# Performance work log

Hardware: AMD Instinct MI355X
Metric: run time of the kernel (lower is better)

The kernel has to match this reference:

```python
import jax, jax.numpy as jnp
import numpy as np

HEADS = 16

def setup_inputs() -> dict:
    key = jax.random.key(0)
    k1, k2, k3, k4 = jax.random.split(key, 4)
    B, T, S, W = 2, 2048, 2048, 1024
    x = jax.random.normal(k1, (B, T, W), dtype=jnp.float32)
    cond_k = jax.random.normal(k2, (B, S, W), dtype=jnp.float32)
    cond_v = jax.random.normal(k3, (B, S, W), dtype=jnp.float32)
    w_proj = jax.random.normal(k4, (W, W), dtype=jnp.float32) * 0.02
    b_proj = jnp.zeros((W,), dtype=jnp.float32)
    return {"x": x, "cond_k": cond_k, "cond_v": cond_v, "w_proj": w_proj, "b_proj": b_proj}

def reference(x, cond_k, cond_v, w_proj, b_proj):
    B, T, W = x.shape
    S = cond_k.shape[1]
    H = HEADS
    d = W // H
    scale = 1.0 / jnp.sqrt(jnp.sqrt(jnp.float32(d)))  # applied to both q and k
    q = x.reshape(B, T, H, d) * scale
    k = cond_k.reshape(B, S, H, d) * scale
    v = cond_v.reshape(B, S, H, d)
    # scores: [B, H, T, S]
    scores = jnp.einsum('bthd,bshd->bhts', q, k)
    w = jax.nn.softmax(scores.astype(jnp.float32), axis=-1).astype(scores.dtype)
    out = jnp.einsum('bhts,bshd->bthd', w, v).reshape(B, T, W)
    # c_proj: torch Linear -> x @ W.T + b
    return out @ w_proj.T + b_proj
```

## Files before the change

kernel.cpp:

```cpp
#include <hip/hip_runtime.h>

#define Bn 2
#define Hn 16
#define Tn 2048
#define Sn 2048
#define Wd 1024
#define Dh 64

typedef __attribute__((ext_vector_type(8))) short s16x8;
typedef __attribute__((ext_vector_type(4))) short s16x4;
typedef __attribute__((ext_vector_type(4))) float f32x4;
typedef __attribute__((ext_vector_type(4))) unsigned u32x4;

#define MFMA(a, b, c) __builtin_amdgcn_mfma_f32_16x16x32_bf16((a), (b), (c), 0, 0, 0)

__device__ __forceinline__ s16x8 ld8(const short* p) { return *(const s16x8*)p; }

__device__ __forceinline__ short f2bf(float f) {
    unsigned u = __builtin_bit_cast(unsigned, f);
    u += 0x7FFFu + ((u >> 16) & 1u);
    return (short)(u >> 16);
}

__device__ __forceinline__ unsigned cvtpk(float lo, float hi) {
    unsigned r;
    asm("v_cvt_pk_bf16_f32 %0, %1, %2" : "=v"(r) : "v"(lo), "v"(hi));
    return r;
}

__device__ __forceinline__ void gl_lds(const short* g, short* lds) {
    __builtin_amdgcn_global_load_lds(
        (const __attribute__((address_space(1))) void*)g,
        (__attribute__((address_space(3))) void*)lds, 16, 0, 0);
}

__global__ __launch_bounds__(256) void prep(const float* __restrict__ ck,
                                            const float* __restrict__ cv,
                                            const float* __restrict__ wp,
                                            short* __restrict__ kp,
                                            short* __restrict__ vp,
                                            short* __restrict__ wb)
{
    __shared__ short T[64][72];
    const int blk = blockIdx.x;
    const int tid = threadIdx.x;
    if (blk < 2048) {
        const int isV = blk >> 10;
        const int c   = blk & 1023;
        const int bh = c >> 5, sc = c & 31;
        const int b = bh >> 4, h = bh & 15;
        const float* src = (isV ? cv : ck) + (size_t)(b * Sn + sc * 64) * Wd + h * Dh;
#pragma unroll
        for (int i = 0; i < 4; ++i) {
            int f = i * 256 + tid, sr = f >> 4, c4 = f & 15;
            float4 v = *(const float4*)(src + (size_t)sr * Wd + c4 * 4);
            s16x4 o;
            o[0] = f2bf(v.x); o[1] = f2bf(v.y); o[2] = f2bf(v.z); o[3] = f2bf(v.w);
            *(s16x4*)&T[sr][c4 * 4] = o;
        }
        __syncthreads();
        const int rt = tid >> 6;
        const int l = tid & 63, quad = l >> 4, l16 = l & 15;
        if (!isV) {
            size_t base = ((size_t)((bh * 128 + sc * 4 + rt) * 2)) * 512 + l * 8;
            *(s16x8*)(kp + base)       = *(const s16x8*)&T[rt * 16 + l16][quad * 8];
            *(s16x8*)(kp + base + 512) = *(const s16x8*)&T[rt * 16 + l16][32 + quad * 8];
        } else {
#pragma unroll
            for (int g = 0; g < 2; ++g) {
                s16x8 o;
#pragma unroll
                for (int j = 0; j < 8; ++j) {
                    int s = 32 * g + 16 * (j >> 2) + quad * 4 + (j & 3);
                    o[j] = T[s][rt * 16 + l16];
                }
                *(s16x8*)(vp + ((size_t)((bh * 32 + sc) * 8 + rt * 2 + g)) * 512 + l * 8) = o;
            }
        }
    } else {
        int i = ((blk - 2048) * 256 + tid) * 8;
        float4 a = *(const float4*)(wp + i);
        float4 b = *(const float4*)(wp + i + 4);
        s16x8 o;
        o[0] = f2bf(a.x); o[1] = f2bf(a.y); o[2] = f2bf(a.z); o[3] = f2bf(a.w);
        o[4] = f2bf(b.x); o[5] = f2bf(b.y); o[6] = f2bf(b.z); o[7] = f2bf(b.w);
        *(s16x8*)(wb + i) = o;
    }
}

__global__ __launch_bounds__(256, 2) void attn_fused(
    const float* __restrict__ x, const short* __restrict__ kp,
    const short* __restrict__ vt, short* __restrict__ ao)
{
    __shared__ alignas(16) short Ks[2][8 * 512];
    __shared__ alignas(16) short Vs[2][8 * 512];

    const int tid  = threadIdx.x;
    const int w    = tid >> 6;
    const int l    = tid & 63;
    const int quad = l >> 4;
    const int l16  = l & 15;

    const int bh = blockIdx.x & 31;
    const int qt = blockIdx.x >> 5;
    const int b  = bh >> 4, h = bh & 15;

    const int qrow0 = qt * 128 + w * 32;

    const short* kp_h = kp + (size_t)bh * 131072;
    const short* vp_h = vt + (size_t)bh * 131072;

    const int f0 = w * 2;

#pragma unroll
    for (int f2 = 0; f2 < 2; ++f2) {
        int f = f0 + f2;
        gl_lds(kp_h + (size_t)f * 512 + l * 8, &Ks[0][f * 512]);
        gl_lds(vp_h + (size_t)f * 512 + l * 8, &Vs[0][f * 512]);
    }

    const float SQ = 0.125f * 1.4426950408889634f;
    s16x8 aq[2][2];
#pragma unroll
    for (int mi = 0; mi < 2; ++mi)
#pragma unroll
        for (int c = 0; c < 2; ++c) {
            const float* p = x + (size_t)(b * Tn + qrow0 + mi * 16 + l16) * Wd
                               + h * Dh + c * 32 + quad * 8;
            float4 a = ((const float4*)p)[0], bb = ((const float4*)p)[1];
            s16x8 o;
            o[0] = f2bf(a.x * SQ); o[1] = f2bf(a.y * SQ); o[2] = f2bf(a.z * SQ); o[3] = f2bf(a.w * SQ);
            o[4] = f2bf(bb.x * SQ); o[5] = f2bf(bb.y * SQ); o[6] = f2bf(bb.z * SQ); o[7] = f2bf(bb.w * SQ);
            aq[mi][c] = o;
        }

    f32x4 oacc[2][4], dnacc[2];
#pragma unroll
    for (int mi = 0; mi < 2; ++mi) {
#pragma unroll
        for (int nt = 0; nt < 4; ++nt) {
            oacc[mi][nt][0] = 0.f; oacc[mi][nt][1] = 0.f;
            oacc[mi][nt][2] = 0.f; oacc[mi][nt][3] = 0.f;
        }
        dnacc[mi][0] = 0.f; dnacc[mi][1] = 0.f; dnacc[mi][2] = 0.f; dnacc[mi][3] = 0.f;
    }

    s16x8 ones;
#pragma unroll
    for (int j = 0; j < 8; ++j) ones[j] = (short)0x3F80;

    const f32x4 z = {0.f, 0.f, 0.f, 0.f};
    const int NIT = Sn / 64;

    asm volatile("s_waitcnt vmcnt(0)" ::: "memory");
    __syncthreads();

    for (int it = 0; it < NIT; ++it) {
        const int p = it & 1;

        if (it + 1 < NIT) {
            const size_t cbase = (size_t)(it + 1) * 8;
#pragma unroll
            for (int f2 = 0; f2 < 2; ++f2) {
                int f = f0 + f2;
                gl_lds(kp_h + (cbase + f) * 512 + l * 8, &Ks[p ^ 1][f * 512]);
                gl_lds(vp_h + (cbase + f) * 512 + l * 8, &Vs[p ^ 1][f * 512]);
            }
        }

        s16x8 kf[4][2];
#pragma unroll
        for (int sj = 0; sj < 4; ++sj)
#pragma unroll
            for (int g = 0; g < 2; ++g)
                kf[sj][g] = *(const s16x8*)&Ks[p][(sj * 2 + g) * 512 + l * 8];

        f32x4 sc[2][4];
        __builtin_amdgcn_s_setprio(1);
#pragma unroll
        for (int sj = 0; sj < 4; ++sj)
#pragma unroll
            for (int mi = 0; mi < 2; ++mi) {
                sc[mi][sj] = MFMA(kf[sj][0], aq[mi][0], z);
                sc[mi][sj] = MFMA(kf[sj][1], aq[mi][1], sc[mi][sj]);
            }
        __builtin_amdgcn_s_setprio(0);

        s16x8 ap[2][2];
#pragma unroll
        for (int mi = 0; mi < 2; ++mi) {
            float ex[4][4];
#pragma unroll
            for (int sj = 0; sj < 4; ++sj)
#pragma unroll
                for (int r = 0; r < 4; ++r)
                    ex[sj][r] = __builtin_amdgcn_exp2f(sc[mi][sj][r]);
#pragma unroll
            for (int g = 0; g < 2; ++g) {
                u32x4 pk;
                pk[0] = cvtpk(ex[2 * g][0],     ex[2 * g][1]);
                pk[1] = cvtpk(ex[2 * g][2],     ex[2 * g][3]);
                pk[2] = cvtpk(ex[2 * g + 1][0], ex[2 * g + 1][1]);
                pk[3] = cvtpk(ex[2 * g + 1][2], ex[2 * g + 1][3]);
                ap[mi][g] = __builtin_bit_cast(s16x8, pk);
            }
        }

        s16x8 vf[4][2];
#pragma unroll
        for (int nt = 0; nt < 4; ++nt)
#pragma unroll
            for (int g = 0; g < 2; ++g)
                vf[nt][g] = *(const s16x8*)&Vs[p][(nt * 2 + g) * 512 + l * 8];

        __builtin_amdgcn_s_setprio(1);
#pragma unroll
        for (int mi = 0; mi < 2; ++mi) {
            dnacc[mi] = MFMA(ap[mi][0], ones, dnacc[mi]);
            dnacc[mi] = MFMA(ap[mi][1], ones, dnacc[mi]);
        }
#pragma unroll
        for (int mi = 0; mi < 2; ++mi)
#pragma unroll
            for (int nt = 0; nt < 4; ++nt) {
                oacc[mi][nt] = MFMA(ap[mi][0], vf[nt][0], oacc[mi][nt]);
                oacc[mi][nt] = MFMA(ap[mi][1], vf[nt][1], oacc[mi][nt]);
            }
        __builtin_amdgcn_s_setprio(0);

        asm volatile("s_waitcnt vmcnt(0)" ::: "memory");
        __syncthreads();
    }

#pragma unroll
    for (int mi = 0; mi < 2; ++mi)
#pragma unroll
        for (int r = 0; r < 4; ++r) {
            float inv = 1.0f / dnacc[mi][r];
            int t = qrow0 + mi * 16 + quad * 4 + r;
#pragma unroll
            for (int nt = 0; nt < 4; ++nt)
                ao[(size_t)(b * Tn + t) * Wd + h * Dh + nt * 16 + l16] =
                    f2bf(oacc[mi][nt][r] * inv);
        }
}

#define LSTR 40

__global__ __launch_bounds__(256, 2) void proj_gemm(
    const short* __restrict__ A, const short* __restrict__ Wb,
    const float* __restrict__ bias, float* __restrict__ out)
{
    __shared__ alignas(16) short As[2][128 * LSTR];
    __shared__ alignas(16) short Bs[2][64 * LSTR];

    const int tid  = threadIdx.x;
    const int w    = tid >> 6;
    const int l    = tid & 63;
    const int quad = l >> 4;
    const int l16  = l & 15;

    const int bn = blockIdx.x & 15;
    const int bm = blockIdx.x >> 4;
    const int m0 = bm * 128;
    const int n0 = bn * 64;
    const int wm = (w & 1) * 64;
    const int wn = (w >> 1) * 32;

    const int rr = tid >> 2;
    const int sg = tid & 3;

    f32x4 acc[4][2];
#pragma unroll
    for (int mi = 0; mi < 4; ++mi)
#pragma unroll
        for (int nt = 0; nt < 2; ++nt) {
            acc[mi][nt][0] = 0.f; acc[mi][nt][1] = 0.f;
            acc[mi][nt][2] = 0.f; acc[mi][nt][3] = 0.f;
        }

    s16x8 ra0 = ld8(A  + (size_t)(m0 + rr) * Wd + sg * 8);
    s16x8 ra1 = ld8(A  + (size_t)(m0 + 64 + rr) * Wd + sg * 8);
    s16x8 rb  = ld8(Wb + (size_t)(n0 + rr) * Wd + sg * 8);
    *(s16x8*)&As[0][rr * LSTR + sg * 8]        = ra0;
    *(s16x8*)&As[0][(rr + 64) * LSTR + sg * 8] = ra1;
    *(s16x8*)&Bs[0][rr * LSTR + sg * 8]        = rb;
    __syncthreads();

    for (int k0 = 0; k0 < Wd; k0 += 32) {
        const int p = (k0 >> 5) & 1;

        if (k0 + 32 < Wd) {
            ra0 = ld8(A  + (size_t)(m0 + rr) * Wd + k0 + 32 + sg * 8);
            ra1 = ld8(A  + (size_t)(m0 + 64 + rr) * Wd + k0 + 32 + sg * 8);
            rb  = ld8(Wb + (size_t)(n0 + rr) * Wd + k0 + 32 + sg * 8);
        }

        s16x8 a[4], bw[2];
#pragma unroll
        for (int mi = 0; mi < 4; ++mi)
            a[mi] = *(const s16x8*)&As[p][(wm + mi * 16 + l16) * LSTR + quad * 8];
#pragma unroll
        for (int nt = 0; nt < 2; ++nt)
            bw[nt] = *(const s16x8*)&Bs[p][(wn + nt * 16 + l16) * LSTR + quad * 8];
        __builtin_amdgcn_s_setprio(1);
#pragma unroll
        for (int mi = 0; mi < 4; ++mi)
#pragma unroll
            for (int nt = 0; nt < 2; ++nt)
                acc[mi][nt] = MFMA(a[mi], bw[nt], acc[mi][nt]);
        __builtin_amdgcn_s_setprio(0);

        if (k0 + 32 < Wd) {
            *(s16x8*)&As[p ^ 1][rr * LSTR + sg * 8]        = ra0;
            *(s16x8*)&As[p ^ 1][(rr + 64) * LSTR + sg * 8] = ra1;
            *(s16x8*)&Bs[p ^ 1][rr * LSTR + sg * 8]        = rb;
        }
        __syncthreads();
    }

#pragma unroll
    for (int nt = 0; nt < 2; ++nt) {
        float bv = bias[n0 + wn + nt * 16 + l16];
#pragma unroll
        for (int mi = 0; mi < 4; ++mi)
#pragma unroll
            for (int r = 0; r < 4; ++r)
                out[(size_t)(m0 + wm + mi * 16 + quad * 4 + r) * Wd + n0 + wn + nt * 16 + l16] =
                    acc[mi][nt][r] + bv;
    }
}

extern "C" void kernel_launch(void* const* d_in, const int* in_sizes, int n_in,
                              void* d_out, int out_size, void* d_ws, size_t ws_size,
                              hipStream_t stream) {
    const float* x  = (const float*)d_in[0];
    const float* ck = (const float*)d_in[1];
    const float* cv = (const float*)d_in[2];
    const float* wp = (const float*)d_in[3];
    const float* bp = (const float*)d_in[4];

    const int nX = Bn * Tn * Wd;
    const int nW = Wd * Wd;

    short* kpb = (short*)d_ws;
    short* vpb = kpb + nX;
    short* wbb = vpb + nX;
    short* am  = wbb + nW;

    prep<<<dim3(2048 + nW / 2048), dim3(256), 0, stream>>>(ck, cv, wp, kpb, vpb, wbb);

    attn_fused<<<dim3(Bn * Hn * (Tn / 128)), dim3(256), 0, stream>>>(x, kpb, vpb, am);
    proj_gemm<<<dim3((Bn * Tn / 128) * (Wd / 64)), dim3(256), 0, stream>>>(
        am, wbb, bp, (float*)d_out);
}
```

Measured before the change: 153.0 us.

## Use 8 waves per attention block with 16 query rows per wave

The attention kernel now launches 512 threads per block. Each of 8 waves owns 16 query rows instead of 32, and each wave loads one K/V fragment per stage instead of two. This halves per-wave register state and raises occupancy to hide LDS and exp latency. In exchange, each K/V fragment read from LDS is reused across only one query tile per wave, so LDS read traffic per MFMA doubles.

```diff
diff --git a/kernel.cpp b/kernel.cpp
--- a/kernel.cpp
+++ b/kernel.cpp
@@ -88,7 +88,7 @@
     }
 }
 
-__global__ __launch_bounds__(256, 2) void attn_fused(
+__global__ __launch_bounds__(512, 4) void attn_fused(
     const float* __restrict__ x, const short* __restrict__ kp,
     const short* __restrict__ vt, short* __restrict__ ao)
 {
@@ -105,45 +105,34 @@
     const int qt = blockIdx.x >> 5;
     const int b  = bh >> 4, h = bh & 15;
 
-    const int qrow0 = qt * 128 + w * 32;
+    const int qrow0 = qt * 128 + w * 16;
 
     const short* kp_h = kp + (size_t)bh * 131072;
     const short* vp_h = vt + (size_t)bh * 131072;
 
-    const int f0 = w * 2;
-
-#pragma unroll
-    for (int f2 = 0; f2 < 2; ++f2) {
-        int f = f0 + f2;
-        gl_lds(kp_h + (size_t)f * 512 + l * 8, &Ks[0][f * 512]);
-        gl_lds(vp_h + (size_t)f * 512 + l * 8, &Vs[0][f * 512]);
-    }
+    gl_lds(kp_h + (size_t)w * 512 + l * 8, &Ks[0][w * 512]);
+    gl_lds(vp_h + (size_t)w * 512 + l * 8, &Vs[0][w * 512]);
 
     const float SQ = 0.125f * 1.4426950408889634f;
-    s16x8 aq[2][2];
-#pragma unroll
-    for (int mi = 0; mi < 2; ++mi)
-#pragma unroll
-        for (int c = 0; c < 2; ++c) {
-            const float* p = x + (size_t)(b * Tn + qrow0 + mi * 16 + l16) * Wd
-                               + h * Dh + c * 32 + quad * 8;
-            float4 a = ((const float4*)p)[0], bb = ((const float4*)p)[1];
-            s16x8 o;
-            o[0] = f2bf(a.x * SQ); o[1] = f2bf(a.y * SQ); o[2] = f2bf(a.z * SQ); o[3] = f2bf(a.w * SQ);
-            o[4] = f2bf(bb.x * SQ); o[5] = f2bf(bb.y * SQ); o[6] = f2bf(bb.z * SQ); o[7] = f2bf(bb.w * SQ);
-            aq[mi][c] = o;
-        }
-
-    f32x4 oacc[2][4], dnacc[2];
-#pragma unroll
-    for (int mi = 0; mi < 2; ++mi) {
-#pragma unroll
-        for (int nt = 0; nt < 4; ++nt) {
-            oacc[mi][nt][0] = 0.f; oacc[mi][nt][1] = 0.f;
-            oacc[mi][nt][2] = 0.f; oacc[mi][nt][3] = 0.f;
-        }
-        dnacc[mi][0] = 0.f; dnacc[mi][1] = 0.f; dnacc[mi][2] = 0.f; dnacc[mi][3] = 0.f;
-    }
+    s16x8 aq[2];
+#pragma unroll
+    for (int c = 0; c < 2; ++c) {
+        const float* p = x + (size_t)(b * Tn + qrow0 + l16) * Wd
+                           + h * Dh + c * 32 + quad * 8;
+        float4 a = ((const float4*)p)[0], bb = ((const float4*)p)[1];
+        s16x8 o;
+        o[0] = f2bf(a.x * SQ); o[1] = f2bf(a.y * SQ); o[2] = f2bf(a.z * SQ); o[3] = f2bf(a.w * SQ);
+        o[4] = f2bf(bb.x * SQ); o[5] = f2bf(bb.y * SQ); o[6] = f2bf(bb.z * SQ); o[7] = f2bf(bb.w * SQ);
+        aq[c] = o;
+    }
+
+    f32x4 oacc[4], dnacc;
+#pragma unroll
+    for (int nt = 0; nt < 4; ++nt) {
+        oacc[nt][0] = 0.f; oacc[nt][1] = 0.f;
+        oacc[nt][2] = 0.f; oacc[nt][3] = 0.f;
+    }
+    dnacc[0] = 0.f; dnacc[1] = 0.f; dnacc[2] = 0.f; dnacc[3] = 0.f;
 
     s16x8 ones;
 #pragma unroll
@@ -160,12 +149,8 @@
 
         if (it + 1 < NIT) {
             const size_t cbase = (size_t)(it + 1) * 8;
-#pragma unroll
-            for (int f2 = 0; f2 < 2; ++f2) {
-                int f = f0 + f2;
-                gl_lds(kp_h + (cbase + f) * 512 + l * 8, &Ks[p ^ 1][f * 512]);
-                gl_lds(vp_h + (cbase + f) * 512 + l * 8, &Vs[p ^ 1][f * 512]);
-            }
+            gl_lds(kp_h + (cbase + w) * 512 + l * 8, &Ks[p ^ 1][w * 512]);
+            gl_lds(vp_h + (cbase + w) * 512 + l * 8, &Vs[p ^ 1][w * 512]);
         }
 
         s16x8 kf[4][2];
@@ -175,26 +160,23 @@
             for (int g = 0; g < 2; ++g)
                 kf[sj][g] = *(const s16x8*)&Ks[p][(sj * 2 + g) * 512 + l * 8];
 
-        f32x4 sc[2][4];
+        f32x4 sc[4];
         __builtin_amdgcn_s_setprio(1);
 #pragma unroll
-        for (int sj = 0; sj < 4; ++sj)
-#pragma unroll
-            for (int mi = 0; mi < 2; ++mi) {
-                sc[mi][sj] = MFMA(kf[sj][0], aq[mi][0], z);
-                sc[mi][sj] = MFMA(kf[sj][1], aq[mi][1], sc[mi][sj]);
-            }
+        for (int sj = 0; sj < 4; ++sj) {
+            sc[sj] = MFMA(kf[sj][0], aq[0], z);
+            sc[sj] = MFMA(kf[sj][1], aq[1], sc[sj]);
+        }
         __builtin_amdgcn_s_setprio(0);
 
-        s16x8 ap[2][2];
-#pragma unroll
-        for (int mi = 0; mi < 2; ++mi) {
+        s16x8 ap[2];
+        {
             float ex[4][4];
 #pragma unroll
             for (int sj = 0; sj < 4; ++sj)
 #pragma unroll
                 for (int r = 0; r < 4; ++r)
-                    ex[sj][r] = __builtin_amdgcn_exp2f(sc[mi][sj][r]);
+                    ex[sj][r] = __builtin_amdgcn_exp2f(sc[sj][r]);
 #pragma unroll
             for (int g = 0; g < 2; ++g) {
                 u32x4 pk;
@@ -202,7 +184,7 @@
                 pk[1] = cvtpk(ex[2 * g][2],     ex[2 * g][3]);
                 pk[2] = cvtpk(ex[2 * g + 1][0], ex[2 * g + 1][1]);
                 pk[3] = cvtpk(ex[2 * g + 1][2], ex[2 * g + 1][3]);
-                ap[mi][g] = __builtin_bit_cast(s16x8, pk);
+                ap[g] = __builtin_bit_cast(s16x8, pk);
             }
         }
 
@@ -214,18 +196,13 @@
                 vf[nt][g] = *(const s16x8*)&Vs[p][(nt * 2 + g) * 512 + l * 8];
 
         __builtin_amdgcn_s_setprio(1);
-#pragma unroll
-        for (int mi = 0; mi < 2; ++mi) {
-            dnacc[mi] = MFMA(ap[mi][0], ones, dnacc[mi]);
-            dnacc[mi] = MFMA(ap[mi][1], ones, dnacc[mi]);
-        }
-#pragma unroll
-        for (int mi = 0; mi < 2; ++mi)
-#pragma unroll
-            for (int nt = 0; nt < 4; ++nt) {
-                oacc[mi][nt] = MFMA(ap[mi][0], vf[nt][0], oacc[mi][nt]);
-                oacc[mi][nt] = MFMA(ap[mi][1], vf[nt][1], oacc[mi][nt]);
-            }
+        dnacc = MFMA(ap[0], ones, dnacc);
+        dnacc = MFMA(ap[1], ones, dnacc);
+#pragma unroll
+        for (int nt = 0; nt < 4; ++nt) {
+            oacc[nt] = MFMA(ap[0], vf[nt][0], oacc[nt]);
+            oacc[nt] = MFMA(ap[1], vf[nt][1], oacc[nt]);
+        }
         __builtin_amdgcn_s_setprio(0);
 
         asm volatile("s_waitcnt vmcnt(0)" ::: "memory");
@@ -233,16 +210,14 @@
     }
 
 #pragma unroll
-    for (int mi = 0; mi < 2; ++mi)
-#pragma unroll
-        for (int r = 0; r < 4; ++r) {
-            float inv = 1.0f / dnacc[mi][r];
-            int t = qrow0 + mi * 16 + quad * 4 + r;
-#pragma unroll
-            for (int nt = 0; nt < 4; ++nt)
-                ao[(size_t)(b * Tn + t) * Wd + h * Dh + nt * 16 + l16] =
-                    f2bf(oacc[mi][nt][r] * inv);
-        }
+    for (int r = 0; r < 4; ++r) {
+        float inv = 1.0f / dnacc[r];
+        int t = qrow0 + quad * 4 + r;
+#pragma unroll
+        for (int nt = 0; nt < 4; ++nt)
+            ao[(size_t)(b * Tn + t) * Wd + h * Dh + nt * 16 + l16] =
+                f2bf(oacc[nt][r] * inv);
+    }
 }
 
 #define LSTR 40
@@ -350,7 +325,7 @@
 
     prep<<<dim3(2048 + nW / 2048), dim3(256), 0, stream>>>(ck, cv, wp, kpb, vpb, wbb);
 
-    attn_fused<<<dim3(Bn * Hn * (Tn / 128)), dim3(256), 0, stream>>>(x, kpb, vpb, am);
+    attn_fused<<<dim3(Bn * Hn * (Tn / 128)), dim3(512), 0, stream>>>(x, kpb, vpb, am);
     proj_gemm<<<dim3((Bn * Tn / 128) * (Wd / 64)), dim3(256), 0, stream>>>(
         am, wbb, bp, (float*)d_out);
 }
```

Result: no change. 154.6 us (+1.1%).

## Split key/value sequence across two wave groups per attention block

Applied to the files above, without the earlier changes.

The attention block doubles to 512 threads. Two groups of four waves each process alternating halves of every 128-key super-chunk into their own LDS buffers. At the end, the second group writes its partial output and denominator to LDS, and the first group adds them, normalizes and writes the result. This is meant to double the resident waves per CU, since the grid only has about two blocks per CU, and so hide more load and MFMA latency. The cost is twice the LDS per block, an extra reduction step and a barrier.

```diff
diff --git a/kernel.cpp b/kernel.cpp
--- a/kernel.cpp
+++ b/kernel.cpp
@@ -88,36 +88,34 @@
     }
 }
 
-__global__ __launch_bounds__(256, 2) void attn_fused(
+__global__ __launch_bounds__(512, 4) void attn_fused(
     const float* __restrict__ x, const short* __restrict__ kp,
     const short* __restrict__ vt, short* __restrict__ ao)
 {
-    __shared__ alignas(16) short Ks[2][8 * 512];
-    __shared__ alignas(16) short Vs[2][8 * 512];
+    __shared__ alignas(16) short Ks[2][2][8 * 512];
+    __shared__ alignas(16) short Vs[2][2][8 * 512];
 
     const int tid  = threadIdx.x;
     const int w    = tid >> 6;
     const int l    = tid & 63;
     const int quad = l >> 4;
     const int l16  = l & 15;
+    const int wq   = w & 3;
+    const int pr   = w >> 2;
 
     const int bh = blockIdx.x & 31;
     const int qt = blockIdx.x >> 5;
     const int b  = bh >> 4, h = bh & 15;
 
-    const int qrow0 = qt * 128 + w * 32;
+    const int qrow0 = qt * 128 + wq * 32;
 
     const short* kp_h = kp + (size_t)bh * 131072;
     const short* vp_h = vt + (size_t)bh * 131072;
 
-    const int f0 = w * 2;
-
-#pragma unroll
-    for (int f2 = 0; f2 < 2; ++f2) {
-        int f = f0 + f2;
-        gl_lds(kp_h + (size_t)f * 512 + l * 8, &Ks[0][f * 512]);
-        gl_lds(vp_h + (size_t)f * 512 + l * 8, &Vs[0][f * 512]);
-    }
+    gl_lds(kp_h + ((size_t)(0 * 8 + w)) * 512 + l * 8, &Ks[0][0][w * 512]);
+    gl_lds(vp_h + ((size_t)(0 * 8 + w)) * 512 + l * 8, &Vs[0][0][w * 512]);
+    gl_lds(kp_h + ((size_t)(1 * 8 + w)) * 512 + l * 8, &Ks[0][1][w * 512]);
+    gl_lds(vp_h + ((size_t)(1 * 8 + w)) * 512 + l * 8, &Vs[0][1][w * 512]);
 
     const float SQ = 0.125f * 1.4426950408889634f;
     s16x8 aq[2][2];
@@ -142,7 +140,8 @@
             oacc[mi][nt][0] = 0.f; oacc[mi][nt][1] = 0.f;
             oacc[mi][nt][2] = 0.f; oacc[mi][nt][3] = 0.f;
         }
-        dnacc[mi][0] = 0.f; dnacc[mi][1] = 0.f; dnacc[mi][2] = 0.f; dnacc[mi][3] = 0.f;
+        dnacc[mi][0] = 0.f; dnacc[mi][1] = 0.f;
+        dnacc[mi][2] = 0.f; dnacc[mi][3] = 0.f;
     }
 
     s16x8 ones;
@@ -150,30 +149,31 @@
     for (int j = 0; j < 8; ++j) ones[j] = (short)0x3F80;
 
     const f32x4 z = {0.f, 0.f, 0.f, 0.f};
-    const int NIT = Sn / 64;
+    const int NSIT = Sn / 128;
 
     asm volatile("s_waitcnt vmcnt(0)" ::: "memory");
     __syncthreads();
 
-    for (int it = 0; it < NIT; ++it) {
-        const int p = it & 1;
-
-        if (it + 1 < NIT) {
-            const size_t cbase = (size_t)(it + 1) * 8;
-#pragma unroll
-            for (int f2 = 0; f2 < 2; ++f2) {
-                int f = f0 + f2;
-                gl_lds(kp_h + (cbase + f) * 512 + l * 8, &Ks[p ^ 1][f * 512]);
-                gl_lds(vp_h + (cbase + f) * 512 + l * 8, &Vs[p ^ 1][f * 512]);
-            }
-        }
+    for (int t = 0; t < NSIT; ++t) {
+        const int sb = t & 1;
+
+        if (t + 1 < NSIT) {
+            const size_t c0 = (size_t)(2 * t + 2) * 8;
+            gl_lds(kp_h + (c0 + w) * 512 + l * 8,     &Ks[sb ^ 1][0][w * 512]);
+            gl_lds(vp_h + (c0 + w) * 512 + l * 8,     &Vs[sb ^ 1][0][w * 512]);
+            gl_lds(kp_h + (c0 + 8 + w) * 512 + l * 8, &Ks[sb ^ 1][1][w * 512]);
+            gl_lds(vp_h + (c0 + 8 + w) * 512 + l * 8, &Vs[sb ^ 1][1][w * 512]);
+        }
+
+        const short* Kb = &Ks[sb][pr][0];
+        const short* Vb = &Vs[sb][pr][0];
 
         s16x8 kf[4][2];
 #pragma unroll
         for (int sj = 0; sj < 4; ++sj)
 #pragma unroll
             for (int g = 0; g < 2; ++g)
-                kf[sj][g] = *(const s16x8*)&Ks[p][(sj * 2 + g) * 512 + l * 8];
+                kf[sj][g] = *(const s16x8*)&Kb[(sj * 2 + g) * 512 + l * 8];
 
         f32x4 sc[2][4];
         __builtin_amdgcn_s_setprio(1);
@@ -211,7 +211,7 @@
         for (int nt = 0; nt < 4; ++nt)
 #pragma unroll
             for (int g = 0; g < 2; ++g)
-                vf[nt][g] = *(const s16x8*)&Vs[p][(nt * 2 + g) * 512 + l * 8];
+                vf[nt][g] = *(const s16x8*)&Vb[(nt * 2 + g) * 512 + l * 8];
 
         __builtin_amdgcn_s_setprio(1);
 #pragma unroll
@@ -232,17 +232,37 @@
         __syncthreads();
     }
 
-#pragma unroll
-    for (int mi = 0; mi < 2; ++mi)
-#pragma unroll
-        for (int r = 0; r < 4; ++r) {
-            float inv = 1.0f / dnacc[mi][r];
-            int t = qrow0 + mi * 16 + quad * 4 + r;
-#pragma unroll
-            for (int nt = 0; nt < 4; ++nt)
-                ao[(size_t)(b * Tn + t) * Wd + h * Dh + nt * 16 + l16] =
-                    f2bf(oacc[mi][nt][r] * inv);
-        }
+    float* ob = (float*)&Ks[0][0][0];
+    float* db = (float*)&Vs[0][0][0];
+    if (pr == 1) {
+#pragma unroll
+        for (int mi = 0; mi < 2; ++mi) {
+#pragma unroll
+            for (int r = 0; r < 4; ++r) {
+                int ql = wq * 32 + mi * 16 + quad * 4 + r;
+#pragma unroll
+                for (int nt = 0; nt < 4; ++nt)
+                    ob[ql * 64 + nt * 16 + l16] = oacc[mi][nt][r];
+                if (l16 == 0) db[ql] = dnacc[mi][r];
+            }
+        }
+    }
+    __syncthreads();
+    if (pr == 0) {
+#pragma unroll
+        for (int mi = 0; mi < 2; ++mi)
+#pragma unroll
+            for (int r = 0; r < 4; ++r) {
+                int ql = wq * 32 + mi * 16 + quad * 4 + r;
+                float inv = 1.0f / (dnacc[mi][r] + db[ql]);
+                int t = qrow0 + mi * 16 + quad * 4 + r;
+#pragma unroll
+                for (int nt = 0; nt < 4; ++nt) {
+                    float v = oacc[mi][nt][r] + ob[ql * 64 + nt * 16 + l16];
+                    ao[(size_t)(b * Tn + t) * Wd + h * Dh + nt * 16 + l16] = f2bf(v * inv);
+                }
+            }
+    }
 }
 
 #define LSTR 40
@@ -350,7 +370,7 @@
 
     prep<<<dim3(2048 + nW / 2048), dim3(256), 0, stream>>>(ck, cv, wp, kpb, vpb, wbb);
 
-    attn_fused<<<dim3(Bn * Hn * (Tn / 128)), dim3(256), 0, stream>>>(x, kpb, vpb, am);
+    attn_fused<<<dim3(Bn * Hn * (Tn / 128)), dim3(512), 0, stream>>>(x, kpb, vpb, am);
     proj_gemm<<<dim3((Bn * Tn / 128) * (Wd / 64)), dim3(256), 0, stream>>>(
         am, wbb, bp, (float*)d_out);
 }
```

Result: no change. 153.8 us (+0.6%).
